# Kernel optimization log

Measured on AMD Instinct MI355X. Metric: run time of the kernel, lower is better.

## Reference

```python
import jax, jax.numpy as jnp
import numpy as np

N, H, W = 2000, 128, 128

def setup_inputs() -> dict:
    key = jax.random.key(0)
    k1, k2, k3, k4 = jax.random.split(key, 4)
    means3D = jax.random.normal(k1, (N, 3), dtype=jnp.float32) * 2.0
    means3D = means3D.at[:, 2].add(10.0)  # put gaussians in front of camera, depth ~in (1,50)
    A = jax.random.normal(k2, (N, 3, 3), dtype=jnp.float32) * 0.1
    covs3d = jnp.einsum('nij,nkj->nik', A, A) + 1e-3 * jnp.eye(3, dtype=jnp.float32)
    colors = jax.random.uniform(k3, (N, 3), dtype=jnp.float32)
    opacities = jax.random.uniform(k4, (N,), dtype=jnp.float32)
    fx = fy = 100.0
    K = jnp.array([[fx, 0.0, W / 2.0], [0.0, fy, H / 2.0], [0.0, 0.0, 1.0]], dtype=jnp.float32)
    R = jnp.eye(3, dtype=jnp.float32)
    t = jnp.zeros((3,), dtype=jnp.float32)
    y, x = jnp.meshgrid(jnp.arange(H, dtype=jnp.float32), jnp.arange(W, dtype=jnp.float32), indexing='ij')
    pixels = jnp.stack([x, y], axis=-1)  # (H, W, 2)
    return {"means3D": means3D, "covs3d": covs3d, "colors": colors,
            "opacities": opacities, "K": K, "R": R, "t": t, "pixels": pixels}

def _render(means3D, covs3d, colors, opacities, K, R, t, pixels):
    # --- projection ---
    cam = means3D @ R.T + t                       # (N,3)
    depths = jnp.clip(cam[:, 2], 1.0, None)       # clamp(min=1.0)
    screen = cam @ K.T
    means2D = screen[:, :2] / screen[:, 2:3]      # (N,2)
    fx, fy = K[0, 0], K[1, 1]
    tx, ty, tz = cam[:, 0], cam[:, 1], cam[:, 2]
    z = jnp.zeros_like(tz)
    J = jnp.stack([jnp.stack([fx / tz, z, -fx * tx / (tz * tz)], -1),
                   jnp.stack([z, fy / tz, -fy * ty / (tz * tz)], -1)], -2)  # (N,2,3)
    covs_cam = jnp.einsum('ij,njk,lk->nil', R, covs3d, R)                   # R C R^T
    covs2D = jnp.einsum('nij,njk,nlk->nil', J, covs_cam, J)                 # (N,2,2)
    valid = (depths > 1.0) & (depths < 50.0)
    # --- depth sort (front to back) ---
    idx = jnp.argsort(depths)
    means2D = means2D[idx]; covs2D = covs2D[idx]
    colors = colors[idx]; opacities = opacities[idx]; valid = valid[idx]
    # --- per-pixel gaussian values ---
    covs2D = covs2D + 1e-4 * jnp.eye(2, dtype=covs2D.dtype)
    a, b = covs2D[:, 0, 0], covs2D[:, 0, 1]
    c, d = covs2D[:, 1, 0], covs2D[:, 1, 1]
    det = a * d - b * c                            # (N,)
    inv = jnp.stack([jnp.stack([d, -b], -1), jnp.stack([-c, a], -1)], -2) / det[:, None, None]
    dx = pixels[None] - means2D[:, None, None, :]  # (N,H,W,2)
    expnum = -jnp.einsum('nhwi,nij,nhwj->nhw', dx, inv, dx)
    gauss = jnp.exp(expnum) / (2.0 * jnp.pi * jnp.sqrt(det))[:, None, None]  # (N,H,W)
    gauss = gauss * valid[:, None, None].astype(gauss.dtype)
    # --- alpha compositing ---
    alphas = opacities[:, None, None] * gauss                   # (N,H,W)
    cum = jnp.cumprod(1.0 - alphas, axis=0)
    trans = jnp.concatenate([jnp.ones((1,) + alphas.shape[1:], alphas.dtype), cum[1:]], axis=0)
    weights = alphas * trans                                    # (N,H,W)
    rendered = jnp.einsum('nhw,nc->hwc', weights, colors)       # (H,W,3)
    return rendered

def reference(means3D, covs3d, colors, opacities, K, R, t, pixels):
    return _render(means3D, covs3d, colors, opacities, K, R, t, pixels)
```

## Files before the change

kernel.cpp:

```cpp
#include <hip/hip_runtime.h>
#include <math.h>

#define NGAUSS 2000
#define IMW 128
#define IMH 128
#define NPIX (IMW*IMH)
#define NW 16
#define SEGSZ ((NGAUSS + NW - 1) / NW)
#define PREPBLK (NGAUSS / NW)

__device__ inline float rdlane(float x, int l) {
    return __uint_as_float(__builtin_amdgcn_readlane(__float_as_uint(x), l));
}

__global__ __launch_bounds__(1024) void preprank_kernel(
    const float* __restrict__ means3D, const float* __restrict__ covs3d,
    const float* __restrict__ colors, const float* __restrict__ opac,
    const float* __restrict__ Km, const float* __restrict__ Rm,
    const float* __restrict__ tv, float* __restrict__ soa)
{
    __shared__ float sdep[2048];

    int tid  = threadIdx.x;
    int lane = tid & 63;
    int w    = tid >> 6;
    int i    = blockIdx.x * NW + w;

    float R0 = Rm[0], R1 = Rm[1], R2 = Rm[2];
    float R3 = Rm[3], R4 = Rm[4], R5 = Rm[5];
    float R6 = Rm[6], R7 = Rm[7], R8 = Rm[8];
    float t0 = tv[0], t1v = tv[1], t2 = tv[2];

    for (int g = tid; g < 2048; g += 1024) {
        float dep = 3.0e38f;
        if (g < NGAUSS) {
            float jx = means3D[3*g+0], jy = means3D[3*g+1], jz = means3D[3*g+2];
            dep = fmaxf(R6*jx + R7*jy + R8*jz + t2, 1.0f);
        }
        sdep[g] = dep;
    }
    __syncthreads();

    float di = sdep[i];
    int rank = 0;
    for (int base = 0; base < 2048; base += 64) {
        int j = base + lane;
        float dj = sdep[j];
        bool lt = (j != i) && ((dj < di) || (dj == di && j < i));
        rank += (int)__popcll(__ballot(lt));
    }

    float mx = means3D[3*i+0], my = means3D[3*i+1], mz = means3D[3*i+2];
    float camx = R0*mx + R1*my + R2*mz + t0;
    float camy = R3*mx + R4*my + R5*mz + t1v;
    float camz = R6*mx + R7*my + R8*mz + t2;
    float depth = fmaxf(camz, 1.0f);
    bool valid = (depth > 1.0f) && (depth < 50.0f);

    float fx = Km[0], cx = Km[2], fy = Km[4], cy = Km[5];
    float invz = 1.0f / camz;
    float m2x = (fx*camx + cx*camz) * invz;
    float m2y = (fy*camy + cy*camz) * invz;
    float J00 = fx*invz, J02 = -fx*camx*invz*invz;
    float J11 = fy*invz, J12 = -fy*camy*invz*invz;

    float S0 = covs3d[9*i+0], S1 = covs3d[9*i+1], S2 = covs3d[9*i+2];
    float S3 = covs3d[9*i+3], S4 = covs3d[9*i+4], S5 = covs3d[9*i+5];
    float S6 = covs3d[9*i+6], S7 = covs3d[9*i+7], S8 = covs3d[9*i+8];

    float RS0 = R0*S0 + R1*S3 + R2*S6;
    float RS1 = R0*S1 + R1*S4 + R2*S7;
    float RS2 = R0*S2 + R1*S5 + R2*S8;
    float RS3 = R3*S0 + R4*S3 + R5*S6;
    float RS4 = R3*S1 + R4*S4 + R5*S7;
    float RS5 = R3*S2 + R4*S5 + R5*S8;
    float RS6 = R6*S0 + R7*S3 + R8*S6;
    float RS7 = R6*S1 + R7*S4 + R8*S7;
    float RS8 = R6*S2 + R7*S5 + R8*S8;

    float Sc0 = RS0*R0 + RS1*R1 + RS2*R2;
    float Sc1 = RS0*R3 + RS1*R4 + RS2*R5;
    float Sc2 = RS0*R6 + RS1*R7 + RS2*R8;
    float Sc3 = RS3*R0 + RS4*R1 + RS5*R2;
    float Sc4 = RS3*R3 + RS4*R4 + RS5*R5;
    float Sc5 = RS3*R6 + RS4*R7 + RS5*R8;
    float Sc6 = RS6*R0 + RS7*R1 + RS8*R2;
    float Sc7 = RS6*R3 + RS7*R4 + RS8*R5;
    float Sc8 = RS6*R6 + RS7*R7 + RS8*R8;

    float A00 = J00*Sc0 + J02*Sc6;
    float A01 = J00*Sc1 + J02*Sc7;
    float A02 = J00*Sc2 + J02*Sc8;
    float A10 = J11*Sc3 + J12*Sc6;
    float A11 = J11*Sc4 + J12*Sc7;
    float A12 = J11*Sc5 + J12*Sc8;

    float a = A00*J00 + A02*J02 + 1e-4f;
    float b = A01*J11 + A02*J12;
    float c = A10*J00 + A12*J02;
    float d = A11*J11 + A12*J12 + 1e-4f;

    float det = a*d - b*c;
    float invdet = 1.0f / det;
    float q0u = d*invdet;
    float q1u = -(b + c)*invdet;
    float q2u = a*invdet;
    float mh = 0.5f*(q0u + q2u);
    float dh = 0.5f*(q0u - q2u);
    float oh = 0.5f*q1u;
    float lmin = mh - sqrtf(dh*dh + oh*oh);
    const float L2E = 1.4426950408889634f;
    float s_cull = lmin * L2E;
    float q0 = -q0u * L2E;
    float q1 = -q1u * L2E;
    float q2 = -q2u * L2E;
    float c0 = opac[i] * 0.15915494309189535f / sqrtf(det);
    if (!valid) { m2x = 0.f; m2y = 0.f; q0 = 0.f; q1 = 0.f; q2 = 0.f; c0 = 0.f; s_cull = 3.0e38f; }

    float cr = colors[3*i+0], cg = colors[3*i+1], cb = colors[3*i+2];
    float v = (lane == 0) ? m2x
            : (lane == 1) ? m2y
            : (lane == 2) ? s_cull
            : (lane == 3) ? q0
            : (lane == 4) ? q1
            : (lane == 5) ? q2
            : (lane == 6) ? c0
            : (lane == 7) ? cr
            : (lane == 8) ? cg
                          : cb;
    if (lane < 10) soa[lane*NGAUSS + rank] = v;
}

__global__ __launch_bounds__(1024) void render_fused(
    const float* __restrict__ soa, float* __restrict__ out)
{
    __shared__ float4 pOut[NW*64];

    int tid  = threadIdx.x;
    int lane = tid & 63;
    int w    = tid >> 6;
    int bid  = blockIdx.x;
    int row  = bid >> 1;
    int xoff = (bid & 1) * 64;

    float px = (float)(xoff + lane);
    float py = (float)row;
    float x0 = (float)xoff, x1 = x0 + 63.0f;

    float Cr = 0.f, Cg = 0.f, Cb = 0.f, T = 1.f;

    int segBase = w * SEGSZ;

    int gA = segBase + lane;
    bool vB = (64 + lane) < SEGSZ;
    int gB = vB ? (segBase + 64 + lane) : segBase;
    float A0 = soa[0*NGAUSS+gA], A1 = soa[1*NGAUSS+gA], A2 = soa[2*NGAUSS+gA];
    float A3 = soa[3*NGAUSS+gA], A4 = soa[4*NGAUSS+gA], A5 = soa[5*NGAUSS+gA];
    float A6 = soa[6*NGAUSS+gA], A7 = soa[7*NGAUSS+gA], A8 = soa[8*NGAUSS+gA];
    float A9 = soa[9*NGAUSS+gA];
    float B0 = soa[0*NGAUSS+gB], B1 = soa[1*NGAUSS+gB], B2 = soa[2*NGAUSS+gB];
    float B3 = soa[3*NGAUSS+gB], B4 = soa[4*NGAUSS+gB], B5 = soa[5*NGAUSS+gB];
    float B6 = soa[6*NGAUSS+gB], B7 = soa[7*NGAUSS+gB], B8 = soa[8*NGAUSS+gB];
    float B9 = soa[9*NGAUSS+gB];

    {
        float dxm = fmaxf(0.f, fmaxf(x0 - A0, A0 - x1));
        float dym = fabsf(py - A1);
        bool keep = A2 * fmaf(dxm, dxm, dym*dym) <= 24.f;
        unsigned long long mask = __ballot(keep);
        while (mask) {
            int b = __builtin_ctzll(mask);
            mask &= mask - 1;
            int gn = segBase + b;
            float gmx = rdlane(A0,b), gmy = rdlane(A1,b);
            float gq0 = rdlane(A3,b), gq1 = rdlane(A4,b), gq2 = rdlane(A5,b);
            float gc0 = rdlane(A6,b), gcr = rdlane(A7,b);
            float gcg = rdlane(A8,b), gcb = rdlane(A9,b);
            float dy = py - gmy;
            float dx = px - gmx;
            float e  = fmaf(fmaf(gq0, dx, gq1*dy), dx, (gq2*dy)*dy);
            float al = gc0 * exp2f(e);
            float wgt = T * al;
            float sel = (gn == 0) ? 0.f : al;
            float f = fmaf(-sel, wgt, wgt);
            Cr = fmaf(f, gcr, Cr);
            Cg = fmaf(f, gcg, Cg);
            Cb = fmaf(f, gcb, Cb);
            T -= wgt;
        }
    }
    {
        float dxm = fmaxf(0.f, fmaxf(x0 - B0, B0 - x1));
        float dym = fabsf(py - B1);
        bool keep = vB && (B2 * fmaf(dxm, dxm, dym*dym) <= 24.f);
        unsigned long long mask = __ballot(keep);
        while (mask) {
            int b = __builtin_ctzll(mask);
            mask &= mask - 1;
            float gmx = rdlane(B0,b), gmy = rdlane(B1,b);
            float gq0 = rdlane(B3,b), gq1 = rdlane(B4,b), gq2 = rdlane(B5,b);
            float gc0 = rdlane(B6,b), gcr = rdlane(B7,b);
            float gcg = rdlane(B8,b), gcb = rdlane(B9,b);
            float dy = py - gmy;
            float dx = px - gmx;
            float e  = fmaf(fmaf(gq0, dx, gq1*dy), dx, (gq2*dy)*dy);
            float al = gc0 * exp2f(e);
            float wgt = T * al;
            float f = fmaf(-al, wgt, wgt);
            Cr = fmaf(f, gcr, Cr);
            Cg = fmaf(f, gcg, Cg);
            Cb = fmaf(f, gcb, Cb);
            T -= wgt;
        }
    }

    pOut[w*64 + lane] = make_float4(Cr, Cg, Cb, T);
    __syncthreads();

    if (tid < 64) {
        float cR = 0.f, cG = 0.f, cB = 0.f, tA = 1.f;
        #pragma unroll
        for (int s = 0; s < NW; ++s) {
            float4 v = pOut[s*64 + tid];
            cR = fmaf(tA, v.x, cR);
            cG = fmaf(tA, v.y, cG);
            cB = fmaf(tA, v.z, cB);
            tA *= v.w;
        }
        int p = row*IMW + xoff + tid;
        out[3*p+0] = cR; out[3*p+1] = cG; out[3*p+2] = cB;
    }
}

extern "C" void kernel_launch(void* const* d_in, const int* in_sizes, int n_in,
                              void* d_out, int out_size, void* d_ws, size_t ws_size,
                              hipStream_t stream)
{
    const float* means3D = (const float*)d_in[0];
    const float* covs3d  = (const float*)d_in[1];
    const float* colors  = (const float*)d_in[2];
    const float* opac    = (const float*)d_in[3];
    const float* Km      = (const float*)d_in[4];
    const float* Rm      = (const float*)d_in[5];
    const float* tv      = (const float*)d_in[6];

    float* soa = (float*)d_ws;

    preprank_kernel<<<PREPBLK, 1024, 0, stream>>>(
        means3D, covs3d, colors, opac, Km, Rm, tv, soa);
    render_fused<<<NPIX/64, 1024, 0, stream>>>(soa, (float*)d_out);
}
```

Measured before the change: 23.79 us.

## Pack gaussian params into float4 AoS and prefetch next kept gaussian

Splits the per-gaussian data into a small SoA holding only the culling fields and a packed float4 array-of-structs for the shading parameters. The render loop no longer holds ten registers per lane and broadcasts them with readlane. Instead it issues uniform float4 loads for each surviving gaussian and software-pipelines the next gaussian's load. The aim is fewer upfront loads, less register pressure and fewer readlane instructions. In exchange, every composited gaussian now costs a memory load, which may add latency on the serial loop's critical path.

```diff
diff --git a/kernel.cpp b/kernel.cpp
--- a/kernel.cpp
+++ b/kernel.cpp
@@ -9,15 +9,12 @@
 #define SEGSZ ((NGAUSS + NW - 1) / NW)
 #define PREPBLK (NGAUSS / NW)
 
-__device__ inline float rdlane(float x, int l) {
-    return __uint_as_float(__builtin_amdgcn_readlane(__float_as_uint(x), l));
-}
-
 __global__ __launch_bounds__(1024) void preprank_kernel(
     const float* __restrict__ means3D, const float* __restrict__ covs3d,
     const float* __restrict__ colors, const float* __restrict__ opac,
     const float* __restrict__ Km, const float* __restrict__ Rm,
-    const float* __restrict__ tv, float* __restrict__ soa)
+    const float* __restrict__ tv,
+    float* __restrict__ soaCull, float4* __restrict__ aos)
 {
     __shared__ float sdep[2048];
 
@@ -118,21 +115,19 @@
     if (!valid) { m2x = 0.f; m2y = 0.f; q0 = 0.f; q1 = 0.f; q2 = 0.f; c0 = 0.f; s_cull = 3.0e38f; }
 
     float cr = colors[3*i+0], cg = colors[3*i+1], cb = colors[3*i+2];
-    float v = (lane == 0) ? m2x
-            : (lane == 1) ? m2y
-            : (lane == 2) ? s_cull
-            : (lane == 3) ? q0
-            : (lane == 4) ? q1
-            : (lane == 5) ? q2
-            : (lane == 6) ? c0
-            : (lane == 7) ? cr
-            : (lane == 8) ? cg
-                          : cb;
-    if (lane < 10) soa[lane*NGAUSS + rank] = v;
+    if (lane < 3) {
+        float4 v = (lane == 0) ? make_float4(m2x, m2y, q0, q1)
+                 : (lane == 1) ? make_float4(q2, c0, cr, cg)
+                               : make_float4(cb, depth, 0.f, 0.f);
+        aos[(size_t)rank*3 + lane] = v;
+        float sv = (lane == 0) ? m2x : (lane == 1) ? m2y : s_cull;
+        soaCull[lane*NGAUSS + rank] = sv;
+    }
 }
 
 __global__ __launch_bounds__(1024) void render_fused(
-    const float* __restrict__ soa, float* __restrict__ out)
+    const float* __restrict__ soaCull, const float4* __restrict__ aos,
+    float* __restrict__ out)
 {
     __shared__ float4 pOut[NW*64];
 
@@ -154,63 +149,51 @@
     int gA = segBase + lane;
     bool vB = (64 + lane) < SEGSZ;
     int gB = vB ? (segBase + 64 + lane) : segBase;
-    float A0 = soa[0*NGAUSS+gA], A1 = soa[1*NGAUSS+gA], A2 = soa[2*NGAUSS+gA];
-    float A3 = soa[3*NGAUSS+gA], A4 = soa[4*NGAUSS+gA], A5 = soa[5*NGAUSS+gA];
-    float A6 = soa[6*NGAUSS+gA], A7 = soa[7*NGAUSS+gA], A8 = soa[8*NGAUSS+gA];
-    float A9 = soa[9*NGAUSS+gA];
-    float B0 = soa[0*NGAUSS+gB], B1 = soa[1*NGAUSS+gB], B2 = soa[2*NGAUSS+gB];
-    float B3 = soa[3*NGAUSS+gB], B4 = soa[4*NGAUSS+gB], B5 = soa[5*NGAUSS+gB];
-    float B6 = soa[6*NGAUSS+gB], B7 = soa[7*NGAUSS+gB], B8 = soa[8*NGAUSS+gB];
-    float B9 = soa[9*NGAUSS+gB];
-
-    {
-        float dxm = fmaxf(0.f, fmaxf(x0 - A0, A0 - x1));
-        float dym = fabsf(py - A1);
-        bool keep = A2 * fmaf(dxm, dxm, dym*dym) <= 24.f;
+    float Amx = soaCull[0*NGAUSS+gA], Amy = soaCull[1*NGAUSS+gA], Asc = soaCull[2*NGAUSS+gA];
+    float Bmx = soaCull[0*NGAUSS+gB], Bmy = soaCull[1*NGAUSS+gB], Bsc = soaCull[2*NGAUSS+gB];
+
+    #pragma unroll
+    for (int chunk = 0; chunk < 2; ++chunk) {
+        int cbase = segBase + chunk*64;
+        float cmx = chunk ? Bmx : Amx;
+        float cmy = chunk ? Bmy : Amy;
+        float csc = chunk ? Bsc : Asc;
+        bool inb = chunk ? vB : true;
+        float dxm = fmaxf(0.f, fmaxf(x0 - cmx, cmx - x1));
+        float dym = fabsf(py - cmy);
+        bool keep = inb && (csc * fmaf(dxm, dxm, dym*dym) <= 24.f);
         unsigned long long mask = __ballot(keep);
-        while (mask) {
-            int b = __builtin_ctzll(mask);
-            mask &= mask - 1;
-            int gn = segBase + b;
-            float gmx = rdlane(A0,b), gmy = rdlane(A1,b);
-            float gq0 = rdlane(A3,b), gq1 = rdlane(A4,b), gq2 = rdlane(A5,b);
-            float gc0 = rdlane(A6,b), gcr = rdlane(A7,b);
-            float gcg = rdlane(A8,b), gcb = rdlane(A9,b);
-            float dy = py - gmy;
-            float dx = px - gmx;
-            float e  = fmaf(fmaf(gq0, dx, gq1*dy), dx, (gq2*dy)*dy);
-            float al = gc0 * exp2f(e);
+        if (!mask) continue;
+
+        int b0 = __builtin_ctzll(mask);
+        int gn = cbase + b0;
+        float4 P0 = aos[(size_t)gn*3+0];
+        float4 P1 = aos[(size_t)gn*3+1];
+        float4 P2 = aos[(size_t)gn*3+2];
+        (void)P2;
+
+        while (true) {
+            unsigned long long m2 = mask & (mask - 1);
+            int b2 = m2 ? __builtin_ctzll(m2) : 0;
+            int gn2 = cbase + b2;
+            float4 N0 = aos[(size_t)gn2*3+0];
+            float4 N1 = aos[(size_t)gn2*3+1];
+            float4 N2 = aos[(size_t)gn2*3+2];
+            (void)N2;
+            float dy = py - P0.y;
+            float dx = px - P0.x;
+            float e  = fmaf(fmaf(P0.z, dx, P0.w*dy), dx, (P1.x*dy)*dy);
+            float al = P1.y * exp2f(e);
             float wgt = T * al;
             float sel = (gn == 0) ? 0.f : al;
             float f = fmaf(-sel, wgt, wgt);
-            Cr = fmaf(f, gcr, Cr);
-            Cg = fmaf(f, gcg, Cg);
-            Cb = fmaf(f, gcb, Cb);
+            Cr = fmaf(f, P1.z, Cr);
+            Cg = fmaf(f, P1.w, Cg);
+            Cb = fmaf(f, P2.x, Cb);
             T -= wgt;
-        }
-    }
-    {
-        float dxm = fmaxf(0.f, fmaxf(x0 - B0, B0 - x1));
-        float dym = fabsf(py - B1);
-        bool keep = vB && (B2 * fmaf(dxm, dxm, dym*dym) <= 24.f);
-        unsigned long long mask = __ballot(keep);
-        while (mask) {
-            int b = __builtin_ctzll(mask);
-            mask &= mask - 1;
-            float gmx = rdlane(B0,b), gmy = rdlane(B1,b);
-            float gq0 = rdlane(B3,b), gq1 = rdlane(B4,b), gq2 = rdlane(B5,b);
-            float gc0 = rdlane(B6,b), gcr = rdlane(B7,b);
-            float gcg = rdlane(B8,b), gcb = rdlane(B9,b);
-            float dy = py - gmy;
-            float dx = px - gmx;
-            float e  = fmaf(fmaf(gq0, dx, gq1*dy), dx, (gq2*dy)*dy);
-            float al = gc0 * exp2f(e);
-            float wgt = T * al;
-            float f = fmaf(-al, wgt, wgt);
-            Cr = fmaf(f, gcr, Cr);
-            Cg = fmaf(f, gcg, Cg);
-            Cb = fmaf(f, gcb, Cb);
-            T -= wgt;
+            mask = m2;
+            if (!mask) break;
+            gn = gn2; P0 = N0; P1 = N1; P2 = N2;
         }
     }
 
@@ -244,9 +227,10 @@
     const float* Rm      = (const float*)d_in[5];
     const float* tv      = (const float*)d_in[6];
 
-    float* soa = (float*)d_ws;
+    float*  soaCull = (float*)d_ws;
+    float4* aos     = (float4*)((float*)d_ws + 6144);
 
     preprank_kernel<<<PREPBLK, 1024, 0, stream>>>(
-        means3D, covs3d, colors, opac, Km, Rm, tv, soa);
-    render_fused<<<NPIX/64, 1024, 0, stream>>>(soa, (float*)d_out);
+        means3D, covs3d, colors, opac, Km, Rm, tv, soaCull, aos);
+    render_fused<<<NPIX/64, 1024, 0, stream>>>(soaCull, aos, (float*)d_out);
 }
```

New measurement: 24.55 us. 1.03x slower.
